# Kernel tuning notes

Measured on AMD Instinct MI355X. Metric: run time of the kernel, lower is better.

## Reference

```python
import jax, jax.numpy as jnp
import numpy as np

B, S, E, H = 2, 2048, 512, 8
D = E // H  # head size = 64
LN_EPS = 1e-5


def setup_inputs() -> dict:
    key = jax.random.key(0)
    ks = jax.random.split(key, 8)
    s_in = 1.0 / np.sqrt(E)
    return {
        "x": jax.random.normal(ks[0], (B, S, E), jnp.float32),
        # per-head projection weights, stored [H, E, D] so q = x @ Wq[h]
        "Wq": jax.random.normal(ks[1], (H, E, D), jnp.float32) * s_in,
        "Wk": jax.random.normal(ks[2], (H, E, D), jnp.float32) * s_in,
        "Wv": jax.random.normal(ks[3], (H, E, D), jnp.float32) * s_in,
        "Wp": jax.random.normal(ks[4], (E, E), jnp.float32) * s_in,
        "bp": jnp.zeros((E,), jnp.float32),
        "gamma": jnp.ones((E,), jnp.float32),
        "beta": jnp.zeros((E,), jnp.float32),
        # causal mask buffer: masked_fill where mask == 0
        "mask": jnp.tril(jnp.ones((S, S), jnp.int32)),
    }


def reference(x, Wq, Wk, Wv, Wp, bp, gamma, beta, mask):
    # batched per-head projections (equivalent to the H small Linears)
    q = jnp.einsum("bse,hed->bhsd", x, Wq)
    k = jnp.einsum("bse,hed->bhsd", x, Wk)
    v = jnp.einsum("bse,hed->bhsd", x, Wv)
    # NOTE: original has NO 1/sqrt(d) scaling
    att_log = jnp.einsum("bhsd,bhtd->bhst", q, k)
    att_log = jnp.where(mask == 0, -jnp.inf, att_log)
    att = jax.nn.softmax(att_log, axis=-1)
    o = jnp.einsum("bhst,bhtd->bhsd", att, v)  # [B,H,S,D]
    # torch.cat((val, values)) prepends each head -> final order head H-1 .. 0
    o = o[:, ::-1]
    vals = o.transpose(0, 2, 1, 3).reshape(B, S, E)
    out = vals @ Wp.T + bp + x
    mu = jnp.mean(out, axis=-1, keepdims=True)
    var = jnp.var(out, axis=-1, keepdims=True)
    return (out - mu) * jax.lax.rsqrt(var + LN_EPS) * gamma + beta
```

## Files before the change

### kernel.cpp

```cpp
#include <hip/hip_runtime.h>

constexpr int Bn = 2;
constexpr int Sn = 2048;
constexpr int En = 512;
constexpr int Hn = 8;
constexpr int Dn = 64;
constexpr int Mn = Bn * Sn;

typedef short bf8 __attribute__((ext_vector_type(8)));
typedef float f32x4 __attribute__((ext_vector_type(4)));

constexpr size_t XY = (size_t)Mn * En;
constexpr size_t WT = (size_t)3 * En * En;
constexpr size_t WP = (size_t)En * En;
constexpr size_t PL = (size_t)Bn * Hn * Sn * Dn;

__device__ __forceinline__ unsigned short f2bf(float f) {
    unsigned int u = __float_as_uint(f);
    unsigned int r = 0x7FFFu + ((u >> 16) & 1u);
    return (unsigned short)((u + r) >> 16);
}
__device__ __forceinline__ float bf2f(unsigned short u) {
    return __uint_as_float(((unsigned int)u) << 16);
}
__device__ __forceinline__ void split2(float f, unsigned short& hi, unsigned short& lo) {
    hi = f2bf(f);
    lo = f2bf(f - bf2f(hi));
}

__device__ __forceinline__ void g2l16(const unsigned short* g, unsigned short* l) {
    typedef __attribute__((address_space(1))) const unsigned int gu32;
    typedef __attribute__((address_space(3))) unsigned int lu32;
    __builtin_amdgcn_global_load_lds((gu32*)(unsigned long long)g,
                                     (lu32*)(unsigned int)(unsigned long long)l,
                                     16, 0, 0);
}

__global__ __launch_bounds__(256)
void prep(const float* __restrict__ x, const float* __restrict__ Wp,
          const float* __restrict__ Wq, const float* __restrict__ Wk,
          const float* __restrict__ Wv,
          unsigned short* __restrict__ xh, unsigned short* __restrict__ xl,
          unsigned short* __restrict__ Wph, unsigned short* __restrict__ Wpl,
          unsigned short* __restrict__ Wth, unsigned short* __restrict__ Wtl)
{
    __shared__ float t[64][65];
    const int bid = blockIdx.x;
    const int tid = threadIdx.x;

    if (bid < 1152) {
        const float* src = (bid < 1024) ? x : Wp;
        unsigned short* hp = (bid < 1024) ? xh : Wph;
        unsigned short* lp = (bid < 1024) ? xl : Wpl;
        const int blk = (bid < 1024) ? bid : (bid - 1024);
        const size_t base = ((size_t)blk * 256 + tid) * 8;
        float a[8];
        *(float4*)&a[0] = *(const float4*)(src + base);
        *(float4*)&a[4] = *(const float4*)(src + base + 4);
        unsigned short h[8], l[8];
        #pragma unroll
        for (int j = 0; j < 8; ++j) split2(a[j], h[j], l[j]);
        *(bf8*)(hp + base) = *(bf8*)&h[0];
        *(bf8*)(lp + base) = *(bf8*)&l[0];
        return;
    }

    const int idx = bid - 1152;
    const int ph = idx >> 3;
    const int proj = ph >> 3, h = ph & 7;
    const int e0 = (idx & 7) * 64;
    const float* W = (proj == 0) ? Wq : (proj == 1) ? Wk : Wv;
    const float* src = W + (size_t)h * En * Dn + (size_t)e0 * Dn;

    const int er = tid >> 2, cg = (tid & 3) * 16;
    #pragma unroll
    for (int c = 0; c < 4; ++c) {
        float4 v = *(const float4*)(src + (size_t)er * Dn + cg + 4 * c);
        t[er][cg + 4 * c + 0] = v.x;
        t[er][cg + 4 * c + 1] = v.y;
        t[er][cg + 4 * c + 2] = v.z;
        t[er][cg + 4 * c + 3] = v.w;
    }
    __syncthreads();

    const int d = tid >> 2, jg = (tid & 3) * 16;
    unsigned short h16[16], l16[16];
    #pragma unroll
    for (int j = 0; j < 16; ++j) split2(t[jg + j][d], h16[j], l16[j]);
    const size_t n = (size_t)proj * 512 + h * 64 + d;
    unsigned short* dh = Wth + n * En + e0 + jg;
    unsigned short* dl = Wtl + n * En + e0 + jg;
    *(bf8*)dh       = *(bf8*)&h16[0];
    *(bf8*)(dh + 8) = *(bf8*)&h16[8];
    *(bf8*)dl       = *(bf8*)&l16[0];
    *(bf8*)(dl + 8) = *(bf8*)&l16[8];
}

__global__ __launch_bounds__(256)
void qkv_gemm(const unsigned short* __restrict__ xh,
              const unsigned short* __restrict__ xl,
              const unsigned short* __restrict__ Wth,
              const unsigned short* __restrict__ Wtl,
              unsigned short* __restrict__ qh_g,
              unsigned short* __restrict__ ql_g,
              unsigned short* __restrict__ kh_g,
              unsigned short* __restrict__ kl_g,
              unsigned short* __restrict__ vT_g)
{
    __shared__ __align__(16) unsigned char smraw[24576];
    unsigned short* ldsAh = (unsigned short*)smraw;
    unsigned short* ldsAl = ldsAh + 4096;
    unsigned short* ldsBh = ldsAl + 4096;
    unsigned short* ldsBl = ldsBh + 2048;
    float (*Cf)[68] = (float(*)[68])(smraw);

    const int tid = threadIdx.x;
    const int m0 = blockIdx.x * 128;
    const int ny = blockIdx.y;
    const int proj = ny >> 3, h = ny & 7;

    const int wave = tid >> 6, lane = tid & 63;
    const int wm = (wave >> 1) * 64, wn = (wave & 1) * 32;
    const int lm = lane & 15, quad = lane >> 4;

    const int l4r = lane >> 2;
    const int l4c = (lane & 3) * 8;
    const unsigned short* gAh0 = xh + (size_t)(m0 + wave * 32 + l4r) * En + l4c;
    const unsigned short* gAh1 = gAh0 + (size_t)16 * En;
    const unsigned short* gAl0 = xl + (size_t)(m0 + wave * 32 + l4r) * En + l4c;
    const unsigned short* gAl1 = gAl0 + (size_t)16 * En;
    const unsigned short* gBh  = Wth + (size_t)(ny * 64 + wave * 16 + l4r) * En + l4c;
    const unsigned short* gBl  = Wtl + (size_t)(ny * 64 + wave * 16 + l4r) * En + l4c;
    unsigned short* dAh0 = ldsAh + wave * 1024;
    unsigned short* dAh1 = dAh0 + 512;
    unsigned short* dAl0 = ldsAl + wave * 1024;
    unsigned short* dAl1 = dAl0 + 512;
    unsigned short* dBh  = ldsBh + wave * 512;
    unsigned short* dBl  = ldsBl + wave * 512;

    f32x4 acc[4][2];
    #pragma unroll
    for (int i = 0; i < 4; ++i)
        #pragma unroll
        for (int j = 0; j < 2; ++j) acc[i][j] = (f32x4){0.f, 0.f, 0.f, 0.f};

    for (int k0 = 0; k0 < En; k0 += 32) {
        g2l16(gAh0 + k0, dAh0);
        g2l16(gAh1 + k0, dAh1);
        g2l16(gAl0 + k0, dAl0);
        g2l16(gAl1 + k0, dAl1);
        g2l16(gBh + k0, dBh);
        g2l16(gBl + k0, dBl);
        __syncthreads();

        bf8 a_h[4], a_l[4], b_h[2], b_l[2];
        #pragma unroll
        for (int mi = 0; mi < 4; ++mi) {
            a_h[mi] = *(const bf8*)(ldsAh + (wm + mi * 16 + lm) * 32 + quad * 8);
            a_l[mi] = *(const bf8*)(ldsAl + (wm + mi * 16 + lm) * 32 + quad * 8);
        }
        #pragma unroll
        for (int ni = 0; ni < 2; ++ni) {
            b_h[ni] = *(const bf8*)(ldsBh + (wn + ni * 16 + lm) * 32 + quad * 8);
            b_l[ni] = *(const bf8*)(ldsBl + (wn + ni * 16 + lm) * 32 + quad * 8);
        }
        #pragma unroll
        for (int mi = 0; mi < 4; ++mi)
            #pragma unroll
            for (int ni = 0; ni < 2; ++ni) {
                acc[mi][ni] = __builtin_amdgcn_mfma_f32_16x16x32_bf16(a_h[mi], b_h[ni], acc[mi][ni], 0, 0, 0);
                acc[mi][ni] = __builtin_amdgcn_mfma_f32_16x16x32_bf16(a_h[mi], b_l[ni], acc[mi][ni], 0, 0, 0);
                acc[mi][ni] = __builtin_amdgcn_mfma_f32_16x16x32_bf16(a_l[mi], b_h[ni], acc[mi][ni], 0, 0, 0);
            }
        __syncthreads();
    }

    if (proj < 2) {
        unsigned short* hp = (proj == 0) ? qh_g : kh_g;
        unsigned short* lp = (proj == 0) ? ql_g : kl_g;
        #pragma unroll
        for (int p = 0; p < 2; ++p) {
            if ((wave >> 1) == p) {
                #pragma unroll
                for (int mi = 0; mi < 4; ++mi)
                    #pragma unroll
                    for (int ni = 0; ni < 2; ++ni)
                        #pragma unroll
                        for (int r = 0; r < 4; ++r)
                            Cf[mi * 16 + quad * 4 + r][wn + ni * 16 + lm] = acc[mi][ni][r];
            }
            __syncthreads();
            {
                const int lr = tid & 63;
                const int cg = (tid >> 6) * 16;
                const int m = m0 + p * 64 + lr;
                const int b = m >> 11, s = m & 2047;
                unsigned short hi[16], lo[16];
                #pragma unroll
                for (int j4 = 0; j4 < 4; ++j4) {
                    float4 v = *(const float4*)&Cf[lr][cg + 4 * j4];
                    split2(v.x, hi[4 * j4 + 0], lo[4 * j4 + 0]);
                    split2(v.y, hi[4 * j4 + 1], lo[4 * j4 + 1]);
                    split2(v.z, hi[4 * j4 + 2], lo[4 * j4 + 2]);
                    split2(v.w, hi[4 * j4 + 3], lo[4 * j4 + 3]);
                }
                const size_t base = (((size_t)(b * Hn + h) * Sn + s) * Dn) + cg;
                *(bf8*)(hp + base)     = *(bf8*)&hi[0];
                *(bf8*)(hp + base + 8) = *(bf8*)&hi[8];
                *(bf8*)(lp + base)     = *(bf8*)&lo[0];
                *(bf8*)(lp + base + 8) = *(bf8*)&lo[8];
            }
            __syncthreads();
        }
    } else {
        #pragma unroll
        for (int mi = 0; mi < 4; ++mi) {
            const int s0 = m0 + wm + mi * 16 + quad * 4;
            const int b = s0 >> 11, s = s0 & 2047;
            #pragma unroll
            for (int ni = 0; ni < 2; ++ni) {
                const int d = wn + ni * 16 + lm;
                ushort4 pk;
                pk.x = f2bf(acc[mi][ni][0]);
                pk.y = f2bf(acc[mi][ni][1]);
                pk.z = f2bf(acc[mi][ni][2]);
                pk.w = f2bf(acc[mi][ni][3]);
                *(ushort4*)(vT_g + ((size_t)(b * Hn + h) * Dn + d) * Sn + s) = pk;
            }
        }
    }
}

__global__ __launch_bounds__(512, 4)
void attn(const unsigned short* __restrict__ qh_g,
          const unsigned short* __restrict__ ql_g,
          const unsigned short* __restrict__ kh_g,
          const unsigned short* __restrict__ kl_g,
          const unsigned short* __restrict__ vT_g,
          unsigned short* __restrict__ Op,
          float* __restrict__ ml)
{
    extern __shared__ unsigned short sm[];
    unsigned short (*khs)[72] = (unsigned short(*)[72])(sm);
    unsigned short (*kls)[72] = (unsigned short(*)[72])(sm + 4608);
    unsigned short (*vTs)[72] = (unsigned short(*)[72])(sm + 9216);
    unsigned short (*pts)[72] = (unsigned short(*)[72])(sm + 13824);
    float* alf = (float*)(sm + 23040);

    const int bidx = blockIdx.x;
    const int xcd = bidx & 7;
    const int g = bidx >> 3;
    const int bh = xcd * 2 + (g & 1);
    const int rest = g >> 1;
    const int hf = rest >> 4;
    const int a_ = rest & 15;
    const int qt = hf ? (15 - a_) : a_;
    const int its = hf ? (qt + 1) : 0;
    const int ite = hf ? (2 * qt + 2) : (qt + 1);

    const int tid = threadIdx.x;
    const int wave = tid >> 6, lane = tid & 63;
    const int quad = lane >> 4, lq = lane & 15;
    const int wq = wave >> 2;
    const int w4 = wave & 3;
    const int qt64 = 2 * qt + wq;
    const int pslot = hf * 512 + bh * 32 + qt64;
    const int dt = qt64;

    const unsigned short* khb = kh_g + (size_t)bh * Sn * Dn;
    const unsigned short* klb = kl_g + (size_t)bh * Sn * Dn;
    const unsigned short* vTb = vT_g + (size_t)bh * Dn * Sn;

    bf8 qfh[2], qfl[2];
    {
        const size_t qoff = ((size_t)bh * Sn + (size_t)qt * 128 + wave * 16 + lq) * Dn;
        #pragma unroll
        for (int c = 0; c < 2; ++c) {
            qfh[c] = *(const bf8*)(qh_g + qoff + c * 32 + quad * 8);
            qfl[c] = *(const bf8*)(ql_g + qoff + c * 32 + quad * 8);
        }
    }

    f32x4 accO[4];
    #pragma unroll
    for (int nj = 0; nj < 4; ++nj) accO[nj] = (f32x4){0.f, 0.f, 0.f, 0.f};
    float m = -1e30f, l = 0.f;

    const int srow = tid & 63;
    const int sdg  = tid >> 6;

    bf8 pk0, pl0, pv0;
    {
        const int t0 = its * 64;
        pk0 = *(const bf8*)(khb + (size_t)(t0 + srow) * Dn + sdg * 8);
        pl0 = *(const bf8*)(klb + (size_t)(t0 + srow) * Dn + sdg * 8);
        pv0 = *(const bf8*)(vTb + (size_t)srow * Sn + t0 + sdg * 8);
    }

    for (int it = its; it < ite; ++it) {
        __syncthreads();
        *(bf8*)&khs[srow][sdg * 8] = pk0;
        *(bf8*)&kls[srow][sdg * 8] = pl0;
        *(bf8*)&vTs[srow][sdg * 8] = pv0;
        __syncthreads();

        if (it + 1 < ite) {
            const int t1 = (it + 1) * 64;
            pk0 = *(const bf8*)(khb + (size_t)(t1 + srow) * Dn + sdg * 8);
            pl0 = *(const bf8*)(klb + (size_t)(t1 + srow) * Dn + sdg * 8);
            pv0 = *(const bf8*)(vTb + (size_t)srow * Sn + t1 + sdg * 8);
        }

        if (it > dt) continue;

        f32x4 accS[4];
        #pragma unroll
        for (int mi = 0; mi < 4; ++mi) accS[mi] = (f32x4){0.f, 0.f, 0.f, 0.f};
        __builtin_amdgcn_s_setprio(1);
        #pragma unroll
        for (int mi = 0; mi < 4; ++mi) {
            #pragma unroll
            for (int c = 0; c < 2; ++c) {
                bf8 ah = *(const bf8*)&khs[mi * 16 + lq][c * 32 + quad * 8];
                bf8 al = *(const bf8*)&kls[mi * 16 + lq][c * 32 + quad * 8];
                accS[mi] = __builtin_amdgcn_mfma_f32_16x16x32_bf16(ah, qfh[c], accS[mi], 0, 0, 0);
                accS[mi] = __builtin_amdgcn_mfma_f32_16x16x32_bf16(ah, qfl[c], accS[mi], 0, 0, 0);
                accS[mi] = __builtin_amdgcn_mfma_f32_16x16x32_bf16(al, qfh[c], accS[mi], 0, 0, 0);
            }
        }
        __builtin_amdgcn_s_setprio(0);

        if (it == dt) {
            const int qrel = w4 * 16 + lq;
            #pragma unroll
            for (int mi = 0; mi < 4; ++mi)
                #pragma unroll
                for (int r = 0; r < 4; ++r)
                    if (mi * 16 + quad * 4 + r > qrel) accS[mi][r] = -INFINITY;
        }

        float mt;
        {
            float t0 = fmaxf(fmaxf(accS[0][0], accS[0][1]), fmaxf(accS[0][2], accS[0][3]));
            float t1 = fmaxf(fmaxf(accS[1][0], accS[1][1]), fmaxf(accS[1][2], accS[1][3]));
            float t2 = fmaxf(fmaxf(accS[2][0], accS[2][1]), fmaxf(accS[2][2], accS[2][3]));
            float t3 = fmaxf(fmaxf(accS[3][0], accS[3][1]), fmaxf(accS[3][2], accS[3][3]));
            mt = fmaxf(fmaxf(t0, t1), fmaxf(t2, t3));
        }
        mt = fmaxf(mt, __shfl_xor(mt, 16));
        mt = fmaxf(mt, __shfl_xor(mt, 32));

        const bool defer = __all(mt <= m + 12.f);
        float mref, alpha = 1.f;
        if (defer) {
            mref = m;
        } else {
            mref = fmaxf(m, mt);
            alpha = __expf(m - mref);
        }

        float ls = 0.f;
        #pragma unroll
        for (int mi = 0; mi < 4; ++mi)
            #pragma unroll
            for (int r = 0; r < 4; ++r) {
                const float p = __expf(accS[mi][r] - mref);
                accS[mi][r] = p;
                ls += p;
            }
        ls += __shfl_xor(ls, 16);
        ls += __shfl_xor(ls, 32);
        if (defer) {
            l += ls;
        } else {
            l = l * alpha + ls;
            m = mref;
        }

        #pragma unroll
        for (int mi = 0; mi < 4; ++mi) {
            ushort4 pk;
            pk.x = f2bf(accS[mi][0]);
            pk.y = f2bf(accS[mi][1]);
            pk.z = f2bf(accS[mi][2]);
            pk.w = f2bf(accS[mi][3]);
            *(ushort4*)&pts[wave * 16 + lq][mi * 16 + quad * 4] = pk;
        }

        if (!defer) {
            if (quad == 0) alf[wave * 16 + lq] = alpha;
            float4 al4 = *(const float4*)&alf[wave * 16 + quad * 4];
            #pragma unroll
            for (int nj = 0; nj < 4; ++nj) {
                accO[nj][0] *= al4.x;
                accO[nj][1] *= al4.y;
                accO[nj][2] *= al4.z;
                accO[nj][3] *= al4.w;
            }
        }

        __builtin_amdgcn_s_setprio(1);
        #pragma unroll
        for (int c = 0; c < 2; ++c) {
            bf8 pf = *(const bf8*)&pts[wave * 16 + lq][c * 32 + quad * 8];
            #pragma unroll
            for (int nj = 0; nj < 4; ++nj) {
                bf8 vf = *(const bf8*)&vTs[nj * 16 + lq][c * 32 + quad * 8];
                accO[nj] = __builtin_amdgcn_mfma_f32_16x16x32_bf16(pf, vf, accO[nj], 0, 0, 0);
            }
        }
        __builtin_amdgcn_s_setprio(0);
    }

    if (quad == 0) {
        const size_t mi_ = ((size_t)pslot * 64 + w4 * 16 + lq) * 2;
        ml[mi_]     = m;
        ml[mi_ + 1] = l;
    }
    #pragma unroll
    for (int r = 0; r < 4; ++r) {
        const int q = w4 * 16 + quad * 4 + r;
        unsigned short* dst = Op + ((size_t)pslot * 64 + q) * 64;
        #pragma unroll
        for (int nj = 0; nj < 4; ++nj)
            dst[nj * 16 + lq] = f2bf(accO[nj][r]);
    }
}

__global__ __launch_bounds__(256)
void out_gemm(const unsigned short* __restrict__ Op,
              const float* __restrict__ ml,
              const unsigned short* __restrict__ Wph,
              const unsigned short* __restrict__ Wpl,
              const float* __restrict__ bp,
              const float* __restrict__ x,
              float* __restrict__ outp,
              float* __restrict__ outp2)
{
    __shared__ unsigned short Ah[64][40], Al[64][40];
    __shared__ __align__(16) unsigned short Bh[128][32], Bl[128][32];

    const int tid = threadIdx.x;
    const int m0 = blockIdx.x * 64;
    const int n0 = blockIdx.y * 128;
    const int kz = blockIdx.z;
    const int kbeg = kz * 256, kend = kbeg + 256;

    const int wave = tid >> 6, lane = tid & 63;
    const int wm = (wave >> 1) * 32, wn = (wave & 1) * 64;
    const int lm = lane & 15, quad = lane >> 4;

    const int am = tid >> 2;
    const int aks = (tid & 3) * 8;
    const int m_row = m0 + am;
    const int b_row = m_row >> 11, s_row = m_row & 2047;
    const int qt = s_row >> 6, qq = s_row & 63;

    float c0[8], c1[8];
    #pragma unroll
    for (int h = 0; h < 8; ++h) {
        const size_t base0 = (((size_t)(b_row * 8 + h) * 32 + qt) * 64 + qq) * 2;
        const size_t base1 = base0 + (size_t)512 * 64 * 2;
        const float m0_ = ml[base0], l0_ = ml[base0 + 1];
        const float m1_ = ml[base1], l1_ = ml[base1 + 1];
        const float mn = fmaxf(m0_, m1_);
        const float a0 = __expf(m0_ - mn), a1 = __expf(m1_ - mn);
        const float inv = 1.f / (a0 * l0_ + a1 * l1_);
        c0[h] = a0 * inv;
        c1[h] = a1 * inv;
    }

    const int l4r = lane >> 2;
    const int l4c = (lane & 3) * 8;
    const unsigned short* gB0h = Wph + (size_t)(n0 + wave * 32 + l4r) * En + l4c;
    const unsigned short* gB1h = gB0h + (size_t)16 * En;
    const unsigned short* gB0l = Wpl + (size_t)(n0 + wave * 32 + l4r) * En + l4c;
    const unsigned short* gB1l = gB0l + (size_t)16 * En;
    unsigned short* dB0h = &Bh[0][0] + wave * 1024;
    unsigned short* dB1h = dB0h + 512;
    unsigned short* dB0l = &Bl[0][0] + wave * 1024;
    unsigned short* dB1l = dB0l + 512;

    f32x4 acc[2][4];
    #pragma unroll
    for (int i = 0; i < 2; ++i)
        #pragma unroll
        for (int j = 0; j < 4; ++j) acc[i][j] = (f32x4){0.f, 0.f, 0.f, 0.f};

    bf8 po0, po1;
    {
        const int e0 = kbeg + aks;
        const int hh = 7 - (e0 >> 6);
        const int dd = e0 & 63;
        const size_t p0 = (((size_t)((b_row * 8 + hh) * 32 + qt)) * 64 + qq) * 64 + dd;
        po0 = *(const bf8*)(Op + p0);
        po1 = *(const bf8*)(Op + p0 + (size_t)512 * 64 * 64);
    }

    for (int k0 = kbeg; k0 < kend; k0 += 32) {
        g2l16(gB0h + k0, dB0h);
        g2l16(gB1h + k0, dB1h);
        g2l16(gB0l + k0, dB0l);
        g2l16(gB1l + k0, dB1l);
        {
            const int h_cur = 7 - ((k0 + aks) >> 6);
            const float w0 = c0[h_cur], w1 = c1[h_cur];
            unsigned short hi[8], lo[8];
            #pragma unroll
            for (int j = 0; j < 8; ++j) {
                const float v = w0 * bf2f((unsigned short)po0[j]) +
                                w1 * bf2f((unsigned short)po1[j]);
                split2(v, hi[j], lo[j]);
            }
            *(bf8*)&Ah[am][aks] = *(bf8*)&hi[0];
            *(bf8*)&Al[am][aks] = *(bf8*)&lo[0];
        }
        __syncthreads();

        if (k0 + 32 < kend) {
            const int e0 = k0 + 32 + aks;
            const int hh = 7 - (e0 >> 6);
            const int dd = e0 & 63;
            const size_t p0 = (((size_t)((b_row * 8 + hh) * 32 + qt)) * 64 + qq) * 64 + dd;
            po0 = *(const bf8*)(Op + p0);
            po1 = *(const bf8*)(Op + p0 + (size_t)512 * 64 * 64);
        }

        bf8 a_h[2], a_l[2], b_h[4], b_l[4];
        #pragma unroll
        for (int mi = 0; mi < 2; ++mi) {
            a_h[mi] = *(const bf8*)&Ah[wm + mi * 16 + lm][quad * 8];
            a_l[mi] = *(const bf8*)&Al[wm + mi * 16 + lm][quad * 8];
        }
        #pragma unroll
        for (int ni = 0; ni < 4; ++ni) {
            b_h[ni] = *(const bf8*)&Bh[wn + ni * 16 + lm][quad * 8];
            b_l[ni] = *(const bf8*)&Bl[wn + ni * 16 + lm][quad * 8];
        }
        #pragma unroll
        for (int mi = 0; mi < 2; ++mi)
            #pragma unroll
            for (int ni = 0; ni < 4; ++ni) {
                acc[mi][ni] = __builtin_amdgcn_mfma_f32_16x16x32_bf16(a_h[mi], b_h[ni], acc[mi][ni], 0, 0, 0);
                acc[mi][ni] = __builtin_amdgcn_mfma_f32_16x16x32_bf16(a_h[mi], b_l[ni], acc[mi][ni], 0, 0, 0);
                acc[mi][ni] = __builtin_amdgcn_mfma_f32_16x16x32_bf16(a_l[mi], b_h[ni], acc[mi][ni], 0, 0, 0);
            }
        __syncthreads();
    }

    float* dst = kz ? outp2 : outp;
    #pragma unroll
    for (int mi = 0; mi < 2; ++mi) {
        #pragma unroll
        for (int r = 0; r < 4; ++r) {
            const int m = m0 + wm + mi * 16 + quad * 4 + r;
            #pragma unroll
            for (int ni = 0; ni < 4; ++ni) {
                const int n = n0 + wn + ni * 16 + lm;
                const size_t idx = (size_t)m * En + n;
                const float extra = kz ? 0.f : (bp[n] + x[idx]);
                dst[idx] = acc[mi][ni][r] + extra;
            }
        }
    }
}

__global__ __launch_bounds__(256)
void ln_kernel(const float* __restrict__ outp,
               const float* __restrict__ outp2,
               const float* __restrict__ gamma,
               const float* __restrict__ beta,
               float* __restrict__ y)
{
    const int row = blockIdx.x * 4 + (threadIdx.x >> 6);
    const int lane = threadIdx.x & 63;
    const size_t off = (size_t)row * En + lane * 8;

    float a[8], b2[8];
    *(float4*)&a[0] = *(const float4*)(outp + off);
    *(float4*)&a[4] = *(const float4*)(outp + off + 4);
    *(float4*)&b2[0] = *(const float4*)(outp2 + off);
    *(float4*)&b2[4] = *(const float4*)(outp2 + off + 4);
    #pragma unroll
    for (int j = 0; j < 8; ++j) a[j] += b2[j];

    float sum = 0.f, sq = 0.f;
    #pragma unroll
    for (int j = 0; j < 8; ++j) { sum += a[j]; sq += a[j] * a[j]; }
    #pragma unroll
    for (int off_ = 1; off_ < 64; off_ <<= 1) {
        sum += __shfl_xor(sum, off_);
        sq  += __shfl_xor(sq, off_);
    }
    const float mu = sum * (1.f / 512.f);
    const float var = sq * (1.f / 512.f) - mu * mu;
    const float rs = rsqrtf(var + 1e-5f);

    const float* g = gamma + lane * 8;
    const float* be = beta + lane * 8;
    float o[8];
    #pragma unroll
    for (int j = 0; j < 8; ++j)
        o[j] = (a[j] - mu) * rs * g[j] + be[j];
    float* yr = y + off;
    *(float4*)(yr)     = *(float4*)&o[0];
    *(float4*)(yr + 4) = *(float4*)&o[4];
}

extern "C" void kernel_launch(void* const* d_in, const int* in_sizes, int n_in,
                              void* d_out, int out_size, void* d_ws, size_t ws_size,
                              hipStream_t stream)
{
    const float* x     = (const float*)d_in[0];
    const float* Wq    = (const float*)d_in[1];
    const float* Wk    = (const float*)d_in[2];
    const float* Wv    = (const float*)d_in[3];
    const float* Wp    = (const float*)d_in[4];
    const float* bp    = (const float*)d_in[5];
    const float* gamma = (const float*)d_in[6];
    const float* beta  = (const float*)d_in[7];

    float* ws   = (float*)d_ws;
    float* ml   = ws;
    float* outp = ws + XY;
    unsigned short* bfb = (unsigned short*)(ws + 2 * XY);
    unsigned short* xh  = bfb;
    unsigned short* xl  = bfb + XY;
    unsigned short* Wth = bfb + 2 * XY;
    unsigned short* Wtl = Wth + WT;
    unsigned short* Wph = Wtl + WT;
    unsigned short* Wpl = Wph + WP;
    unsigned short* qh  = Wpl + WP;
    unsigned short* ql  = qh + PL;
    unsigned short* kh  = ql + PL;
    unsigned short* kl  = kh + PL;
    unsigned short* vT  = kl + PL;
    unsigned short* Op = xh;
    float* outp2 = (float*)qh;

    const int attn_lds = 46592;
    hipFuncSetAttribute((const void*)attn,
                        hipFuncAttributeMaxDynamicSharedMemorySize, attn_lds);

    prep<<<dim3(1344), 256, 0, stream>>>(x, Wp, Wq, Wk, Wv,
                                         xh, xl, Wph, Wpl, Wth, Wtl);
    qkv_gemm<<<dim3(Mn / 128, 24), 256, 0, stream>>>(xh, xl, Wth, Wtl,
                                                     qh, ql, kh, kl, vT);
    attn<<<dim3(512), 512, attn_lds, stream>>>(qh, ql, kh, kl, vT, Op, ml);
    out_gemm<<<dim3(Mn / 64, En / 128, 2), 256, 0, stream>>>(Op, ml, Wph, Wpl,
                                                             bp, x, outp, outp2);
    ln_kernel<<<dim3(Mn / 4), 256, 0, stream>>>(outp, outp2, gamma, beta,
                                                (float*)d_out);
}
```

Measured before the change: 173.9 us.

## Double-buffer QKV GEMM LDS tiles and merge attention causal halves per block

The QKV projection GEMM now double-buffers its LDS tiles and prefetches the next k-slice before computing the current one, which drops one barrier per iteration and overlaps loads with MFMA work. The attention kernel now launches 256 blocks instead of 512, and each block handles both balanced halves of the causal work (a q tile and its mirror) one after the other. The aim is to cut launch and tail imbalance and to hide GEMM load latency. In exchange, the GEMM doubles its LDS use, which may lower occupancy, and attention has fewer blocks to spread across the CUs.

Measured after the change: 172.2 us. No clear change (-1.0%).

```diff
diff --git a/kernel.cpp b/kernel.cpp
--- a/kernel.cpp
+++ b/kernel.cpp
@@ -107,11 +107,11 @@
               unsigned short* __restrict__ kl_g,
               unsigned short* __restrict__ vT_g)
 {
-    __shared__ __align__(16) unsigned char smraw[24576];
+    __shared__ __align__(16) unsigned char smraw[49152];
     unsigned short* ldsAh = (unsigned short*)smraw;
-    unsigned short* ldsAl = ldsAh + 4096;
-    unsigned short* ldsBh = ldsAl + 4096;
-    unsigned short* ldsBl = ldsBh + 2048;
+    unsigned short* ldsAl = ldsAh + 8192;
+    unsigned short* ldsBh = ldsAl + 8192;
+    unsigned short* ldsBl = ldsBh + 4096;
     float (*Cf)[68] = (float(*)[68])(smraw);
 
     const int tid = threadIdx.x;
@@ -131,12 +131,8 @@
     const unsigned short* gAl1 = gAl0 + (size_t)16 * En;
     const unsigned short* gBh  = Wth + (size_t)(ny * 64 + wave * 16 + l4r) * En + l4c;
     const unsigned short* gBl  = Wtl + (size_t)(ny * 64 + wave * 16 + l4r) * En + l4c;
-    unsigned short* dAh0 = ldsAh + wave * 1024;
-    unsigned short* dAh1 = dAh0 + 512;
-    unsigned short* dAl0 = ldsAl + wave * 1024;
-    unsigned short* dAl1 = dAl0 + 512;
-    unsigned short* dBh  = ldsBh + wave * 512;
-    unsigned short* dBl  = ldsBl + wave * 512;
+    const int offA = wave * 1024;
+    const int offB = wave * 512;
 
     f32x4 acc[4][2];
     #pragma unroll
@@ -144,25 +140,40 @@
         #pragma unroll
         for (int j = 0; j < 2; ++j) acc[i][j] = (f32x4){0.f, 0.f, 0.f, 0.f};
 
+    g2l16(gAh0, ldsAh + offA);
+    g2l16(gAh1, ldsAh + offA + 512);
+    g2l16(gAl0, ldsAl + offA);
+    g2l16(gAl1, ldsAl + offA + 512);
+    g2l16(gBh,  ldsBh + offB);
+    g2l16(gBl,  ldsBl + offB);
+
+    int cur = 0;
     for (int k0 = 0; k0 < En; k0 += 32) {
-        g2l16(gAh0 + k0, dAh0);
-        g2l16(gAh1 + k0, dAh1);
-        g2l16(gAl0 + k0, dAl0);
-        g2l16(gAl1 + k0, dAl1);
-        g2l16(gBh + k0, dBh);
-        g2l16(gBl + k0, dBl);
         __syncthreads();
-
+        const int nxt = cur ^ 1;
+        if (k0 + 32 < En) {
+            g2l16(gAh0 + k0 + 32, ldsAh + nxt * 4096 + offA);
+            g2l16(gAh1 + k0 + 32, ldsAh + nxt * 4096 + offA + 512);
+            g2l16(gAl0 + k0 + 32, ldsAl + nxt * 4096 + offA);
+            g2l16(gAl1 + k0 + 32, ldsAl + nxt * 4096 + offA + 512);
+            g2l16(gBh + k0 + 32,  ldsBh + nxt * 2048 + offB);
+            g2l16(gBl + k0 + 32,  ldsBl + nxt * 2048 + offB);
+        }
+
+        const unsigned short* bAh = ldsAh + cur * 4096;
+        const unsigned short* bAl = ldsAl + cur * 4096;
+        const unsigned short* bBh = ldsBh + cur * 2048;
+        const unsigned short* bBl = ldsBl + cur * 2048;
         bf8 a_h[4], a_l[4], b_h[2], b_l[2];
         #pragma unroll
         for (int mi = 0; mi < 4; ++mi) {
-            a_h[mi] = *(const bf8*)(ldsAh + (wm + mi * 16 + lm) * 32 + quad * 8);
-            a_l[mi] = *(const bf8*)(ldsAl + (wm + mi * 16 + lm) * 32 + quad * 8);
+            a_h[mi] = *(const bf8*)(bAh + (wm + mi * 16 + lm) * 32 + quad * 8);
+            a_l[mi] = *(const bf8*)(bAl + (wm + mi * 16 + lm) * 32 + quad * 8);
         }
         #pragma unroll
         for (int ni = 0; ni < 2; ++ni) {
-            b_h[ni] = *(const bf8*)(ldsBh + (wn + ni * 16 + lm) * 32 + quad * 8);
-            b_l[ni] = *(const bf8*)(ldsBl + (wn + ni * 16 + lm) * 32 + quad * 8);
+            b_h[ni] = *(const bf8*)(bBh + (wn + ni * 16 + lm) * 32 + quad * 8);
+            b_l[ni] = *(const bf8*)(bBl + (wn + ni * 16 + lm) * 32 + quad * 8);
         }
         #pragma unroll
         for (int mi = 0; mi < 4; ++mi)
@@ -172,8 +183,9 @@
                 acc[mi][ni] = __builtin_amdgcn_mfma_f32_16x16x32_bf16(a_h[mi], b_l[ni], acc[mi][ni], 0, 0, 0);
                 acc[mi][ni] = __builtin_amdgcn_mfma_f32_16x16x32_bf16(a_l[mi], b_h[ni], acc[mi][ni], 0, 0, 0);
             }
-        __syncthreads();
-    }
+        cur = nxt;
+    }
+    __syncthreads();
 
     if (proj < 2) {
         unsigned short* hp = (proj == 0) ? qh_g : kh_g;
@@ -251,179 +263,181 @@
     const int xcd = bidx & 7;
     const int g = bidx >> 3;
     const int bh = xcd * 2 + (g & 1);
-    const int rest = g >> 1;
-    const int hf = rest >> 4;
-    const int a_ = rest & 15;
-    const int qt = hf ? (15 - a_) : a_;
-    const int its = hf ? (qt + 1) : 0;
-    const int ite = hf ? (2 * qt + 2) : (qt + 1);
+    const int qp = g >> 1;
 
     const int tid = threadIdx.x;
     const int wave = tid >> 6, lane = tid & 63;
     const int quad = lane >> 4, lq = lane & 15;
     const int wq = wave >> 2;
     const int w4 = wave & 3;
-    const int qt64 = 2 * qt + wq;
-    const int pslot = hf * 512 + bh * 32 + qt64;
-    const int dt = qt64;
 
     const unsigned short* khb = kh_g + (size_t)bh * Sn * Dn;
     const unsigned short* klb = kl_g + (size_t)bh * Sn * Dn;
     const unsigned short* vTb = vT_g + (size_t)bh * Dn * Sn;
 
-    bf8 qfh[2], qfl[2];
-    {
-        const size_t qoff = ((size_t)bh * Sn + (size_t)qt * 128 + wave * 16 + lq) * Dn;
-        #pragma unroll
-        for (int c = 0; c < 2; ++c) {
-            qfh[c] = *(const bf8*)(qh_g + qoff + c * 32 + quad * 8);
-            qfl[c] = *(const bf8*)(ql_g + qoff + c * 32 + quad * 8);
-        }
-    }
-
-    f32x4 accO[4];
-    #pragma unroll
-    for (int nj = 0; nj < 4; ++nj) accO[nj] = (f32x4){0.f, 0.f, 0.f, 0.f};
-    float m = -1e30f, l = 0.f;
-
     const int srow = tid & 63;
     const int sdg  = tid >> 6;
 
-    bf8 pk0, pl0, pv0;
-    {
-        const int t0 = its * 64;
-        pk0 = *(const bf8*)(khb + (size_t)(t0 + srow) * Dn + sdg * 8);
-        pl0 = *(const bf8*)(klb + (size_t)(t0 + srow) * Dn + sdg * 8);
-        pv0 = *(const bf8*)(vTb + (size_t)srow * Sn + t0 + sdg * 8);
-    }
-
-    for (int it = its; it < ite; ++it) {
-        __syncthreads();
-        *(bf8*)&khs[srow][sdg * 8] = pk0;
-        *(bf8*)&kls[srow][sdg * 8] = pl0;
-        *(bf8*)&vTs[srow][sdg * 8] = pv0;
-        __syncthreads();
-
-        if (it + 1 < ite) {
-            const int t1 = (it + 1) * 64;
-            pk0 = *(const bf8*)(khb + (size_t)(t1 + srow) * Dn + sdg * 8);
-            pl0 = *(const bf8*)(klb + (size_t)(t1 + srow) * Dn + sdg * 8);
-            pv0 = *(const bf8*)(vTb + (size_t)srow * Sn + t1 + sdg * 8);
-        }
-
-        if (it > dt) continue;
-
-        f32x4 accS[4];
-        #pragma unroll
-        for (int mi = 0; mi < 4; ++mi) accS[mi] = (f32x4){0.f, 0.f, 0.f, 0.f};
-        __builtin_amdgcn_s_setprio(1);
-        #pragma unroll
-        for (int mi = 0; mi < 4; ++mi) {
+    #pragma unroll 1
+    for (int ph = 0; ph < 2; ++ph) {
+        const int qt  = ph ? (15 - qp) : qp;
+        const int its = ph ? (qt + 1) : 0;
+        const int ite = ph ? (2 * qt + 2) : (qt + 1);
+        const int qt64 = 2 * qt + wq;
+        const int pslot = ph * 512 + bh * 32 + qt64;
+        const int dt = qt64;
+
+        bf8 qfh[2], qfl[2];
+        {
+            const size_t qoff = ((size_t)bh * Sn + (size_t)qt * 128 + wave * 16 + lq) * Dn;
             #pragma unroll
             for (int c = 0; c < 2; ++c) {
-                bf8 ah = *(const bf8*)&khs[mi * 16 + lq][c * 32 + quad * 8];
-                bf8 al = *(const bf8*)&kls[mi * 16 + lq][c * 32 + quad * 8];
-                accS[mi] = __builtin_amdgcn_mfma_f32_16x16x32_bf16(ah, qfh[c], accS[mi], 0, 0, 0);
-                accS[mi] = __builtin_amdgcn_mfma_f32_16x16x32_bf16(ah, qfl[c], accS[mi], 0, 0, 0);
-                accS[mi] = __builtin_amdgcn_mfma_f32_16x16x32_bf16(al, qfh[c], accS[mi], 0, 0, 0);
-            }
-        }
-        __builtin_amdgcn_s_setprio(0);
-
-        if (it == dt) {
-            const int qrel = w4 * 16 + lq;
+                qfh[c] = *(const bf8*)(qh_g + qoff + c * 32 + quad * 8);
+                qfl[c] = *(const bf8*)(ql_g + qoff + c * 32 + quad * 8);
+            }
+        }
+
+        f32x4 accO[4];
+        #pragma unroll
+        for (int nj = 0; nj < 4; ++nj) accO[nj] = (f32x4){0.f, 0.f, 0.f, 0.f};
+        float m = -1e30f, l = 0.f;
+
+        bf8 pk0, pl0, pv0;
+        {
+            const int t0 = its * 64;
+            pk0 = *(const bf8*)(khb + (size_t)(t0 + srow) * Dn + sdg * 8);
+            pl0 = *(const bf8*)(klb + (size_t)(t0 + srow) * Dn + sdg * 8);
+            pv0 = *(const bf8*)(vTb + (size_t)srow * Sn + t0 + sdg * 8);
+        }
+
+        for (int it = its; it < ite; ++it) {
+            __syncthreads();
+            *(bf8*)&khs[srow][sdg * 8] = pk0;
+            *(bf8*)&kls[srow][sdg * 8] = pl0;
+            *(bf8*)&vTs[srow][sdg * 8] = pv0;
+            __syncthreads();
+
+            if (it + 1 < ite) {
+                const int t1 = (it + 1) * 64;
+                pk0 = *(const bf8*)(khb + (size_t)(t1 + srow) * Dn + sdg * 8);
+                pl0 = *(const bf8*)(klb + (size_t)(t1 + srow) * Dn + sdg * 8);
+                pv0 = *(const bf8*)(vTb + (size_t)srow * Sn + t1 + sdg * 8);
+            }
+
+            if (it > dt) continue;
+
+            f32x4 accS[4];
+            #pragma unroll
+            for (int mi = 0; mi < 4; ++mi) accS[mi] = (f32x4){0.f, 0.f, 0.f, 0.f};
+            __builtin_amdgcn_s_setprio(1);
+            #pragma unroll
+            for (int mi = 0; mi < 4; ++mi) {
+                #pragma unroll
+                for (int c = 0; c < 2; ++c) {
+                    bf8 ah = *(const bf8*)&khs[mi * 16 + lq][c * 32 + quad * 8];
+                    bf8 al = *(const bf8*)&kls[mi * 16 + lq][c * 32 + quad * 8];
+                    accS[mi] = __builtin_amdgcn_mfma_f32_16x16x32_bf16(ah, qfh[c], accS[mi], 0, 0, 0);
+                    accS[mi] = __builtin_amdgcn_mfma_f32_16x16x32_bf16(ah, qfl[c], accS[mi], 0, 0, 0);
+                    accS[mi] = __builtin_amdgcn_mfma_f32_16x16x32_bf16(al, qfh[c], accS[mi], 0, 0, 0);
+                }
+            }
+            __builtin_amdgcn_s_setprio(0);
+
+            if (it == dt) {
+                const int qrel = w4 * 16 + lq;
+                #pragma unroll
+                for (int mi = 0; mi < 4; ++mi)
+                    #pragma unroll
+                    for (int r = 0; r < 4; ++r)
+                        if (mi * 16 + quad * 4 + r > qrel) accS[mi][r] = -INFINITY;
+            }
+
+            float mt;
+            {
+                float t0 = fmaxf(fmaxf(accS[0][0], accS[0][1]), fmaxf(accS[0][2], accS[0][3]));
+                float t1 = fmaxf(fmaxf(accS[1][0], accS[1][1]), fmaxf(accS[1][2], accS[1][3]));
+                float t2 = fmaxf(fmaxf(accS[2][0], accS[2][1]), fmaxf(accS[2][2], accS[2][3]));
+                float t3 = fmaxf(fmaxf(accS[3][0], accS[3][1]), fmaxf(accS[3][2], accS[3][3]));
+                mt = fmaxf(fmaxf(t0, t1), fmaxf(t2, t3));
+            }
+            mt = fmaxf(mt, __shfl_xor(mt, 16));
+            mt = fmaxf(mt, __shfl_xor(mt, 32));
+
+            const bool defer = __all(mt <= m + 12.f);
+            float mref, alpha = 1.f;
+            if (defer) {
+                mref = m;
+            } else {
+                mref = fmaxf(m, mt);
+                alpha = __expf(m - mref);
+            }
+
+            float ls = 0.f;
             #pragma unroll
             for (int mi = 0; mi < 4; ++mi)
                 #pragma unroll
-                for (int r = 0; r < 4; ++r)
-                    if (mi * 16 + quad * 4 + r > qrel) accS[mi][r] = -INFINITY;
-        }
-
-        float mt;
-        {
-            float t0 = fmaxf(fmaxf(accS[0][0], accS[0][1]), fmaxf(accS[0][2], accS[0][3]));
-            float t1 = fmaxf(fmaxf(accS[1][0], accS[1][1]), fmaxf(accS[1][2], accS[1][3]));
-            float t2 = fmaxf(fmaxf(accS[2][0], accS[2][1]), fmaxf(accS[2][2], accS[2][3]));
-            float t3 = fmaxf(fmaxf(accS[3][0], accS[3][1]), fmaxf(accS[3][2], accS[3][3]));
-            mt = fmaxf(fmaxf(t0, t1), fmaxf(t2, t3));
-        }
-        mt = fmaxf(mt, __shfl_xor(mt, 16));
-        mt = fmaxf(mt, __shfl_xor(mt, 32));
-
-        const bool defer = __all(mt <= m + 12.f);
-        float mref, alpha = 1.f;
-        if (defer) {
-            mref = m;
-        } else {
-            mref = fmaxf(m, mt);
-            alpha = __expf(m - mref);
-        }
-
-        float ls = 0.f;
-        #pragma unroll
-        for (int mi = 0; mi < 4; ++mi)
-            #pragma unroll
-            for (int r = 0; r < 4; ++r) {
-                const float p = __expf(accS[mi][r] - mref);
-                accS[mi][r] = p;
-                ls += p;
-            }
-        ls += __shfl_xor(ls, 16);
-        ls += __shfl_xor(ls, 32);
-        if (defer) {
-            l += ls;
-        } else {
-            l = l * alpha + ls;
-            m = mref;
-        }
-
-        #pragma unroll
-        for (int mi = 0; mi < 4; ++mi) {
-            ushort4 pk;
-            pk.x = f2bf(accS[mi][0]);
-            pk.y = f2bf(accS[mi][1]);
-            pk.z = f2bf(accS[mi][2]);
-            pk.w = f2bf(accS[mi][3]);
-            *(ushort4*)&pts[wave * 16 + lq][mi * 16 + quad * 4] = pk;
-        }
-
-        if (!defer) {
-            if (quad == 0) alf[wave * 16 + lq] = alpha;
-            float4 al4 = *(const float4*)&alf[wave * 16 + quad * 4];
-            #pragma unroll
-            for (int nj = 0; nj < 4; ++nj) {
-                accO[nj][0] *= al4.x;
-                accO[nj][1] *= al4.y;
-                accO[nj][2] *= al4.z;
-                accO[nj][3] *= al4.w;
-            }
-        }
-
-        __builtin_amdgcn_s_setprio(1);
-        #pragma unroll
-        for (int c = 0; c < 2; ++c) {
-            bf8 pf = *(const bf8*)&pts[wave * 16 + lq][c * 32 + quad * 8];
-            #pragma unroll
-            for (int nj = 0; nj < 4; ++nj) {
-                bf8 vf = *(const bf8*)&vTs[nj * 16 + lq][c * 32 + quad * 8];
-                accO[nj] = __builtin_amdgcn_mfma_f32_16x16x32_bf16(pf, vf, accO[nj], 0, 0, 0);
-            }
-        }
-        __builtin_amdgcn_s_setprio(0);
-    }
-
-    if (quad == 0) {
-        const size_t mi_ = ((size_t)pslot * 64 + w4 * 16 + lq) * 2;
-        ml[mi_]     = m;
-        ml[mi_ + 1] = l;
-    }
-    #pragma unroll
-    for (int r = 0; r < 4; ++r) {
-        const int q = w4 * 16 + quad * 4 + r;
-        unsigned short* dst = Op + ((size_t)pslot * 64 + q) * 64;
-        #pragma unroll
-        for (int nj = 0; nj < 4; ++nj)
-            dst[nj * 16 + lq] = f2bf(accO[nj][r]);
+                for (int r = 0; r < 4; ++r) {
+                    const float p = __expf(accS[mi][r] - mref);
+                    accS[mi][r] = p;
+                    ls += p;
+                }
+            ls += __shfl_xor(ls, 16);
+            ls += __shfl_xor(ls, 32);
+            if (defer) {
+                l += ls;
+            } else {
+                l = l * alpha + ls;
+                m = mref;
+            }
+
+            #pragma unroll
+            for (int mi = 0; mi < 4; ++mi) {
+                ushort4 pk;
+                pk.x = f2bf(accS[mi][0]);
+                pk.y = f2bf(accS[mi][1]);
+                pk.z = f2bf(accS[mi][2]);
+                pk.w = f2bf(accS[mi][3]);
+                *(ushort4*)&pts[wave * 16 + lq][mi * 16 + quad * 4] = pk;
+            }
+
+            if (!defer) {
+                if (quad == 0) alf[wave * 16 + lq] = alpha;
+                float4 al4 = *(const float4*)&alf[wave * 16 + quad * 4];
+                #pragma unroll
+                for (int nj = 0; nj < 4; ++nj) {
+                    accO[nj][0] *= al4.x;
+                    accO[nj][1] *= al4.y;
+                    accO[nj][2] *= al4.z;
+                    accO[nj][3] *= al4.w;
+                }
+            }
+
+            __builtin_amdgcn_s_setprio(1);
+            #pragma unroll
+            for (int c = 0; c < 2; ++c) {
+                bf8 pf = *(const bf8*)&pts[wave * 16 + lq][c * 32 + quad * 8];
+                #pragma unroll
+                for (int nj = 0; nj < 4; ++nj) {
+                    bf8 vf = *(const bf8*)&vTs[nj * 16 + lq][c * 32 + quad * 8];
+                    accO[nj] = __builtin_amdgcn_mfma_f32_16x16x32_bf16(pf, vf, accO[nj], 0, 0, 0);
+                }
+            }
+            __builtin_amdgcn_s_setprio(0);
+        }
+
+        if (quad == 0) {
+            const size_t mi_ = ((size_t)pslot * 64 + w4 * 16 + lq) * 2;
+            ml[mi_]     = m;
+            ml[mi_ + 1] = l;
+        }
+        #pragma unroll
+        for (int r = 0; r < 4; ++r) {
+            const int q = w4 * 16 + quad * 4 + r;
+            unsigned short* dst = Op + ((size_t)pslot * 64 + q) * 64;
+            #pragma unroll
+            for (int nj = 0; nj < 4; ++nj)
+                dst[nj * 16 + lq] = f2bf(accO[nj][r]);
+        }
     }
 }
 
@@ -646,7 +660,7 @@
                                          xh, xl, Wph, Wpl, Wth, Wtl);
     qkv_gemm<<<dim3(Mn / 128, 24), 256, 0, stream>>>(xh, xl, Wth, Wtl,
                                                      qh, ql, kh, kl, vT);
-    attn<<<dim3(512), 512, attn_lds, stream>>>(qh, ql, kh, kl, vT, Op, ml);
+    attn<<<dim3(256), 512, attn_lds, stream>>>(qh, ql, kh, kl, vT, Op, ml);
     out_gemm<<<dim3(Mn / 64, En / 128, 2), 256, 0, stream>>>(Op, ml, Wph, Wpl,
                                                              bp, x, outp, outp2);
     ln_kernel<<<dim3(Mn / 4), 256, 0, stream>>>(outp, outp2, gamma, beta,
```
